# Performance work log

Measured on AMD Instinct MI355X. Metric: run time of the kernel, lower is better.

The kernel has to match this reference:

```python
import jax, jax.numpy as jnp
import numpy as np

EMBED_DIM = 512
NUM_HEADS = 8
HEAD_DIM = EMBED_DIM // NUM_HEADS


def setup_inputs() -> dict:
    key = jax.random.key(0)
    ks = jax.random.split(key, 9)
    C = EMBED_DIM
    s = 1.0 / np.sqrt(C)
    x = jax.random.normal(ks[0], (1, 4096, C), dtype=jnp.float32)
    Wq = jax.random.uniform(ks[1], (C, C), jnp.float32, -s, s)
    bq = jax.random.uniform(ks[2], (C,), jnp.float32, -s, s)
    Wk = jax.random.uniform(ks[3], (C, C), jnp.float32, -s, s)
    bk = jax.random.uniform(ks[4], (C,), jnp.float32, -s, s)
    Wv = jax.random.uniform(ks[5], (C, C), jnp.float32, -s, s)
    bv = jax.random.uniform(ks[6], (C,), jnp.float32, -s, s)
    Wo = jax.random.uniform(ks[7], (C, C), jnp.float32, -s, s)
    bo = jax.random.uniform(ks[8], (C,), jnp.float32, -s, s)
    return {"x": x, "Wq": Wq, "bq": bq, "Wk": Wk, "bk": bk,
            "Wv": Wv, "bv": bv, "Wo": Wo, "bo": bo}


def reference(x, Wq, bq, Wk, bk, Wv, bv, Wo, bo):
    B, N, C = x.shape
    H, D = NUM_HEADS, HEAD_DIM
    # QKV projections, split into heads: [B, H, N, D]
    def proj(W, b):
        y = x @ W + b
        return y.reshape(B, N, H, D).transpose(0, 2, 1, 3)
    Q, K, V = proj(Wq, bq), proj(Wk, bk), proj(Wv, bv)
    # NOTE: original scales by 1/sqrt(embed_dim), NOT 1/sqrt(head_dim)
    scale = 1.0 / jnp.sqrt(jnp.float32(C)).astype(x.dtype)
    scores = jnp.einsum('bhnd,bhmd->bhnm', Q, K) * scale  # [B,H,N,N]
    attn = jax.nn.softmax(scores, axis=-1)
    out = jnp.einsum('bhnm,bhmd->bhnd', attn, V)  # [B,H,N,D]
    out = out.transpose(0, 2, 1, 3).reshape(B, N, C)
    return out @ Wo + bo
```

## Files before the change

kernel.cpp:

```cpp
#include <hip/hip_runtime.h>
#include <hip/hip_bf16.h>

#define SEQ 4096
#define CDIM 512
#define NHEAD 8
#define HDIM 64
#define KVB 64
#define NSPLIT 4
#define TILES_PER_SPLIT (SEQ / KVB / NSPLIT)

typedef __attribute__((ext_vector_type(8))) short bf16x8;
typedef __attribute__((ext_vector_type(4))) float f32x4;
typedef __attribute__((ext_vector_type(16))) float f32x16;

__device__ __forceinline__ short f2b(float f) {
  union { float f; unsigned u; } v; v.f = f;
  unsigned u = v.u;
  unsigned r = u + 0x7fffu + ((u >> 16) & 1u);
  return (short)(r >> 16);
}
__device__ __forceinline__ float b2f(short s) {
  union { unsigned u; float f; } v; v.u = ((unsigned)(unsigned short)s) << 16;
  return v.f;
}
__device__ __forceinline__ unsigned pk2(float a, float b) {
  union { __hip_bfloat162 h; unsigned u; } z;
  z.h = __float22bfloat162_rn(make_float2(a, b));
  return z.u;
}

__global__ __launch_bounds__(256) void prep_kernel(
    const float* __restrict__ x,
    const float* __restrict__ Wq, const float* __restrict__ Wk,
    const float* __restrict__ Wv, const float* __restrict__ Wo,
    short* __restrict__ xb,
    short* __restrict__ Wqt, short* __restrict__ Wkt,
    short* __restrict__ Wvt, short* __restrict__ Wot) {
  __shared__ short tile[32][33];
  int b = blockIdx.x, tid = threadIdx.x;
  if (b < 2048) {
    int i = (b * 256 + tid) * 4;
    float4 v = *(const float4*)(x + i);
    short4 o;
    o.x = f2b(v.x); o.y = f2b(v.y); o.z = f2b(v.z); o.w = f2b(v.w);
    *(short4*)(xb + i) = o;
    return;
  }
  int t = b - 2048;
  int mat = t >> 8; t &= 255;
  const float* W = mat == 0 ? Wq : mat == 1 ? Wk : mat == 2 ? Wv : Wo;
  short* Wt = mat == 0 ? Wqt : mat == 1 ? Wkt : mat == 2 ? Wvt : Wot;
  int n0 = (t & 15) * 32, k0 = (t >> 4) * 32;
  int tx = tid & 31, ty = tid >> 5;
  for (int i = 0; i < 32; i += 8)
    tile[ty + i][tx] = f2b(W[(size_t)(k0 + ty + i) * CDIM + n0 + tx]);
  __syncthreads();
  for (int i = 0; i < 32; i += 8)
    Wt[(size_t)(n0 + ty + i) * CDIM + k0 + tx] = tile[tx][ty + i];
}

__global__ __launch_bounds__(256) void qkv_gemm_kernel(
    const short* __restrict__ A,
    const short* __restrict__ Wqt, const short* __restrict__ Wkt, const short* __restrict__ Wvt,
    const float* __restrict__ bq, const float* __restrict__ bk, const float* __restrict__ bv,
    short* __restrict__ Qb, short* __restrict__ Kb, short* __restrict__ Vtb) {
  __shared__ short As[64 * 64];
  __shared__ short Bs[64 * 64];
  const int z = blockIdx.z;
  const short* Bt = z == 0 ? Wqt : z == 1 ? Wkt : Wvt;
  const float* bias = z == 0 ? bq : z == 1 ? bk : bv;
  const int m0 = blockIdx.x * 64, n0 = blockIdx.y * 64;
  const int tid = threadIdx.x;
  const int w = tid >> 6, lane = tid & 63, g = lane >> 4, l16 = lane & 15;
  f32x4 acc[4] = {};
  for (int kt = 0; kt < CDIM; kt += 64) {
    __syncthreads();
    for (int it = 0; it < 2; ++it) {
      int c = tid + it * 256;
      int r = c >> 3, cc = (c & 7) * 8;
      int sw = r * 64 + (cc ^ ((r & 7) * 8));
      *(bf16x8*)(As + sw) = *(const bf16x8*)(A + (size_t)(m0 + r) * CDIM + kt + cc);
      *(bf16x8*)(Bs + sw) = *(const bf16x8*)(Bt + (size_t)(n0 + r) * CDIM + kt + cc);
    }
    __syncthreads();
    const int ar = w * 16 + l16;
    for (int ks = 0; ks < 2; ++ks) {
      int c0 = ks * 32 + 8 * g;
      bf16x8 af = *(const bf16x8*)(As + ar * 64 + (c0 ^ ((ar & 7) * 8)));
      for (int ni = 0; ni < 4; ++ni) {
        int br = ni * 16 + l16;
        bf16x8 bf = *(const bf16x8*)(Bs + br * 64 + (c0 ^ ((br & 7) * 8)));
        acc[ni] = __builtin_amdgcn_mfma_f32_16x16x32_bf16(af, bf, acc[ni], 0, 0, 0);
      }
    }
  }
  for (int ni = 0; ni < 4; ++ni) {
    int col = n0 + ni * 16 + l16;
    float bv_ = bias[col];
    for (int j = 0; j < 4; ++j) {
      int row = m0 + w * 16 + g * 4 + j;
      float v = acc[ni][j] + bv_;
      if (z == 0)      Qb[(size_t)row * CDIM + col] = f2b(v);
      else if (z == 1) Kb[(size_t)row * CDIM + col] = f2b(v);
      else             Vtb[(size_t)col * SEQ + row] = f2b(v);
    }
  }
}

__global__ __launch_bounds__(256) void out_gemm_kernel(
    const short* __restrict__ A, const short* __restrict__ Bt,
    const float* __restrict__ bias, float* __restrict__ out) {
  __shared__ short As[64 * 64];
  __shared__ short Bs[64 * 64];
  const int m0 = blockIdx.x * 64, n0 = blockIdx.y * 64;
  const int tid = threadIdx.x;
  const int w = tid >> 6, lane = tid & 63, g = lane >> 4, l16 = lane & 15;
  f32x4 acc[4] = {};
  for (int kt = 0; kt < CDIM; kt += 64) {
    __syncthreads();
    for (int it = 0; it < 2; ++it) {
      int c = tid + it * 256;
      int r = c >> 3, cc = (c & 7) * 8;
      int sw = r * 64 + (cc ^ ((r & 7) * 8));
      *(bf16x8*)(As + sw) = *(const bf16x8*)(A + (size_t)(m0 + r) * CDIM + kt + cc);
      *(bf16x8*)(Bs + sw) = *(const bf16x8*)(Bt + (size_t)(n0 + r) * CDIM + kt + cc);
    }
    __syncthreads();
    const int ar = w * 16 + l16;
    for (int ks = 0; ks < 2; ++ks) {
      int c0 = ks * 32 + 8 * g;
      bf16x8 af = *(const bf16x8*)(As + ar * 64 + (c0 ^ ((ar & 7) * 8)));
      for (int ni = 0; ni < 4; ++ni) {
        int br = ni * 16 + l16;
        bf16x8 bf = *(const bf16x8*)(Bs + br * 64 + (c0 ^ ((br & 7) * 8)));
        acc[ni] = __builtin_amdgcn_mfma_f32_16x16x32_bf16(af, bf, acc[ni], 0, 0, 0);
      }
    }
  }
  for (int ni = 0; ni < 4; ++ni) {
    int col = n0 + ni * 16 + l16;
    float bv_ = bias[col];
    for (int j = 0; j < 4; ++j) {
      int row = m0 + w * 16 + g * 4 + j;
      out[(size_t)row * CDIM + col] = acc[ni][j] + bv_;
    }
  }
}

__global__ __launch_bounds__(512, 4) void attn_kernel(
    const short* __restrict__ Qb,
    const short* __restrict__ Kb,
    const short* __restrict__ Vtb,
    short* __restrict__ Op0, short* __restrict__ Op1,
    short* __restrict__ Op2, short* __restrict__ Op3,
    float* __restrict__ lpart) {
  __shared__ __align__(16) char arena[33792];
  __shared__ float lzp[4][32];
  short* KsB = (short*)arena;
  short* VsB = (short*)(arena + 16384);
  const int bid = blockIdx.x;
  const int h = bid & 7;
  const int rest = bid >> 3;
  const int split = rest & 3;
  const int q0 = (rest >> 2) * 128;
  const int kvbase = split * (TILES_PER_SPLIT * KVB);
  const int tid = threadIdx.x;
  const int wid = tid >> 6, lane = tid & 63;
  const int l31 = lane & 31, hi = lane >> 5;
  const int rh = wid >> 1, kq = wid & 1;
  const float scale2 = 0.06375872274f;

  short* Opart = split == 0 ? Op0 : split == 1 ? Op1 : split == 2 ? Op2 : Op3;

  bf16x8 qf[4];
  {
    int qrow = q0 + rh * 32 + l31;
#pragma unroll
    for (int kst = 0; kst < 4; ++kst) {
      bf16x8 q = *(const bf16x8*)(Qb + (size_t)qrow * CDIM + h * 64 + kst * 16 + hi * 8);
#pragma unroll
      for (int i = 0; i < 8; ++i) q[i] = f2b(b2f(q[i]) * scale2);
      qf[kst] = q;
    }
  }

  const int srow = tid >> 3;
  const int scol8 = 8 * ((tid & 7) ^ (srow & 7));
  auto stage = [&](int buf, int kv0) {
    __builtin_amdgcn_global_load_lds(
        (const __attribute__((address_space(1))) void*)(
            Kb + (size_t)(kv0 + srow) * CDIM + h * 64 + scol8),
        (__attribute__((address_space(3))) void*)(&KsB[buf * 4096 + tid * 8]), 16, 0, 0);
    __builtin_amdgcn_global_load_lds(
        (const __attribute__((address_space(1))) void*)(
            Vtb + (size_t)(h * 64 + srow) * SEQ + kv0 + scol8),
        (__attribute__((address_space(3))) void*)(&VsB[buf * 4096 + tid * 8]), 16, 0, 0);
  };

  f32x16 osum[2] = {};
  float lsum = 0.f;

  stage(0, kvbase);
  __syncthreads();

  int cur = 0;
  for (int t = 0; t < TILES_PER_SPLIT; ++t) {
    if (t + 1 < TILES_PER_SPLIT) stage(cur ^ 1, kvbase + (t + 1) * KVB);

    const short* ks_lds = KsB + cur * 4096;
    const short* vs_lds = VsB + cur * 4096;

    f32x16 s = {};
    __builtin_amdgcn_s_setprio(1);
#pragma unroll
    for (int kst = 0; kst < 4; ++kst) {
      int row = kq * 32 + l31;
      bf16x8 kf = *(const bf16x8*)(ks_lds + row * 64 + ((kst * 16 + hi * 8) ^ ((row & 7) * 8)));
      s = __builtin_amdgcn_mfma_f32_32x32x16_bf16(kf, qf[kst], s, 0, 0, 0);
    }
    __builtin_amdgcn_s_setprio(0);

    unsigned w[8];
    float ls0 = 0.f, ls1 = 0.f;
#pragma unroll
    for (int m = 0; m < 8; ++m) {
      float p0 = __builtin_amdgcn_exp2f(s[2 * m]);
      float p1 = __builtin_amdgcn_exp2f(s[2 * m + 1]);
      ls0 += p0; ls1 += p1;
      w[m] = pk2(p0, p1);
    }
    lsum += ls0 + ls1;

#pragma unroll
    for (int ks2 = 0; ks2 < 2; ++ks2) {
      union { unsigned u[4]; bf16x8 v; } pf;
#if __has_builtin(__builtin_amdgcn_permlane32_swap)
      {
        auto sw0 = __builtin_amdgcn_permlane32_swap(w[4 * ks2 + 0], w[4 * ks2 + 2], false, false);
        auto sw1 = __builtin_amdgcn_permlane32_swap(w[4 * ks2 + 1], w[4 * ks2 + 3], false, false);
        pf.u[0] = sw0[0]; pf.u[1] = sw1[0]; pf.u[2] = sw0[1]; pf.u[3] = sw1[1];
      }
#else
      {
        unsigned t0 = hi ? w[4 * ks2 + 0] : w[4 * ks2 + 2];
        unsigned t1 = hi ? w[4 * ks2 + 1] : w[4 * ks2 + 3];
        unsigned r0 = __shfl_xor(t0, 32);
        unsigned r1 = __shfl_xor(t1, 32);
        pf.u[0] = hi ? r0 : w[4 * ks2 + 0];
        pf.u[1] = hi ? r1 : w[4 * ks2 + 1];
        pf.u[2] = hi ? w[4 * ks2 + 2] : r0;
        pf.u[3] = hi ? w[4 * ks2 + 3] : r1;
      }
#endif
      __builtin_amdgcn_s_setprio(1);
#pragma unroll
      for (int dm = 0; dm < 2; ++dm) {
        int vrow = dm * 32 + l31;
        bf16x8 vf = *(const bf16x8*)(
            vs_lds + vrow * 64 + ((kq * 32 + ks2 * 16 + hi * 8) ^ ((vrow & 7) * 8)));
        osum[dm] = __builtin_amdgcn_mfma_f32_32x32x16_bf16(vf, pf.v, osum[dm], 0, 0, 0);
      }
      __builtin_amdgcn_s_setprio(0);
    }

    __syncthreads();
    cur ^= 1;
  }

  lsum += __shfl_xor(lsum, 32);

  __syncthreads();
  float* bufA = (float*)arena;
#define OD(dm, r) ((dm) * 32 + ((r) & 3) + 8 * ((r) >> 2) + 4 * hi)
#define OADDR(dm, r) (rh * 2112 + OD(dm, r) * 33 + l31)
  if (kq == 1) {
    if (hi == 0) lzp[rh][l31] = lsum;
#pragma unroll
    for (int dm = 0; dm < 2; ++dm)
#pragma unroll
      for (int r = 0; r < 16; ++r) bufA[OADDR(dm, r)] = osum[dm][r];
  }
  __syncthreads();
  if (kq == 0) {
#pragma unroll
    for (int dm = 0; dm < 2; ++dm)
#pragma unroll
      for (int r = 0; r < 16; ++r) {
        float v = osum[dm][r] + bufA[OADDR(dm, r)];
        bufA[OADDR(dm, r)] = v;
      }
    float lt = lsum + lzp[rh][l31];
    if (hi == 0)
      lpart[(size_t)(split * NHEAD + h) * SEQ + q0 + rh * 32 + l31] = lt;
  }
  __syncthreads();
#undef OD
#undef OADDR

  {
    int q_ = tid >> 2;
    int dc = (tid & 3) * 16;
    int qr = q_ >> 5, ql = q_ & 31;
    short ov[16];
#pragma unroll
    for (int i = 0; i < 16; ++i)
      ov[i] = f2b(bufA[qr * 2112 + (dc + i) * 33 + ql]);
    *(bf16x8*)(Opart + (size_t)(q0 + q_) * CDIM + h * 64 + dc) = *(bf16x8*)(ov);
    *(bf16x8*)(Opart + (size_t)(q0 + q_) * CDIM + h * 64 + dc + 8) = *(bf16x8*)(ov + 8);
  }
}

__global__ __launch_bounds__(256) void combine_kernel(
    const short* __restrict__ p0, const short* __restrict__ p1,
    const short* __restrict__ p2, const short* __restrict__ p3,
    const float* __restrict__ lpart, short* __restrict__ Ab) {
  int t = blockIdx.x * 256 + threadIdx.x;
  size_t base = (size_t)t * 8;
  int q = (int)(base >> 9), c = (int)(base & 511), h = c >> 6;
  float l = lpart[(size_t)(0 * NHEAD + h) * SEQ + q] +
            lpart[(size_t)(1 * NHEAD + h) * SEQ + q] +
            lpart[(size_t)(2 * NHEAD + h) * SEQ + q] +
            lpart[(size_t)(3 * NHEAD + h) * SEQ + q];
  float rinv = 1.f / l;
  bf16x8 a0 = *(const bf16x8*)(p0 + base);
  bf16x8 a1 = *(const bf16x8*)(p1 + base);
  bf16x8 a2 = *(const bf16x8*)(p2 + base);
  bf16x8 a3 = *(const bf16x8*)(p3 + base);
  short ov[8];
#pragma unroll
  for (int i = 0; i < 8; ++i)
    ov[i] = f2b((b2f(a0[i]) + b2f(a1[i]) + b2f(a2[i]) + b2f(a3[i])) * rinv);
  *(bf16x8*)(Ab + base) = *(bf16x8*)(ov);
}

extern "C" void kernel_launch(void* const* d_in, const int* in_sizes, int n_in,
                              void* d_out, int out_size, void* d_ws, size_t ws_size,
                              hipStream_t stream) {
  const float* x  = (const float*)d_in[0];
  const float* Wq = (const float*)d_in[1];
  const float* bq = (const float*)d_in[2];
  const float* Wk = (const float*)d_in[3];
  const float* bk = (const float*)d_in[4];
  const float* Wv = (const float*)d_in[5];
  const float* bv = (const float*)d_in[6];
  const float* Wo = (const float*)d_in[7];
  const float* bo = (const float*)d_in[8];
  float* out = (float*)d_out;

  short* ws = (short*)d_ws;
  size_t off = 0;
  short* xb  = ws + off; off += (size_t)SEQ * CDIM;
  short* Wqt = ws + off; off += (size_t)CDIM * CDIM;
  short* Wkt = ws + off; off += (size_t)CDIM * CDIM;
  short* Wvt = ws + off; off += (size_t)CDIM * CDIM;
  short* Wot = ws + off; off += (size_t)CDIM * CDIM;
  short* Qb  = ws + off; off += (size_t)SEQ * CDIM;
  short* Kb  = ws + off; off += (size_t)SEQ * CDIM;
  short* Vtb = ws + off; off += (size_t)CDIM * SEQ;
  short* Ab  = ws + off; off += (size_t)SEQ * CDIM;
  short* Op1 = ws + off; off += (size_t)SEQ * CDIM;
  short* Op2 = ws + off; off += (size_t)SEQ * CDIM;
  short* Op3 = ws + off; off += (size_t)SEQ * CDIM;
  float* lpart = (float*)(ws + off); off += (size_t)NSPLIT * NHEAD * SEQ * 2;
  short* Op0 = xb;

  prep_kernel<<<2048 + 4 * 256, 256, 0, stream>>>(x, Wq, Wk, Wv, Wo, xb, Wqt, Wkt, Wvt, Wot);
  qkv_gemm_kernel<<<dim3(SEQ / 64, CDIM / 64, 3), 256, 0, stream>>>(
      xb, Wqt, Wkt, Wvt, bq, bk, bv, Qb, Kb, Vtb);
  attn_kernel<<<(SEQ / 128) * NHEAD * NSPLIT, 512, 0, stream>>>(
      Qb, Kb, Vtb, Op0, Op1, Op2, Op3, lpart);
  combine_kernel<<<SEQ * CDIM / 8 / 256, 256, 0, stream>>>(Op0, Op1, Op2, Op3, lpart, Ab);
  out_gemm_kernel<<<dim3(SEQ / 64, CDIM / 64), 256, 0, stream>>>(Ab, Wot, bo, out);
}
```

Measured before the change: 88.72 us.

## Software-pipeline attention loop: overlap QK^T of next tile with PV of current

Restructures the attention KV loop so that each phase issues the QK^T MFMAs for tile t+1 alongside the PV MFMAs for tile t. The exp2/softmax for the new scores is computed after the MFMAs are issued, so it can overlap with them. This needs K/V staging to move from double to triple LDS buffering, with a prologue that computes the first scores and an epilogue that does the last PV. Staging addresses are now advanced incrementally by pointer bumps instead of being recomputed each time. The larger LDS footprint (48KB arena) may lower the number of resident blocks per CU below the requested four.

```diff
diff --git a/kernel.cpp b/kernel.cpp
--- a/kernel.cpp
+++ b/kernel.cpp
@@ -154,10 +154,10 @@
     short* __restrict__ Op0, short* __restrict__ Op1,
     short* __restrict__ Op2, short* __restrict__ Op3,
     float* __restrict__ lpart) {
-  __shared__ __align__(16) char arena[33792];
+  __shared__ __align__(16) char arena[49152];
   __shared__ float lzp[4][32];
   short* KsB = (short*)arena;
-  short* VsB = (short*)(arena + 16384);
+  short* VsB = (short*)(arena + 24576);
   const int bid = blockIdx.x;
   const int h = bid & 7;
   const int rest = bid >> 3;
@@ -186,41 +186,24 @@
 
   const int srow = tid >> 3;
   const int scol8 = 8 * ((tid & 7) ^ (srow & 7));
-  auto stage = [&](int buf, int kv0) {
+  const short* kstage = Kb + (size_t)(kvbase + srow) * CDIM + h * 64 + scol8;
+  const short* vstage = Vtb + (size_t)(h * 64 + srow) * SEQ + kvbase + scol8;
+  auto stage = [&](short* sK, short* sV) {
     __builtin_amdgcn_global_load_lds(
-        (const __attribute__((address_space(1))) void*)(
-            Kb + (size_t)(kv0 + srow) * CDIM + h * 64 + scol8),
-        (__attribute__((address_space(3))) void*)(&KsB[buf * 4096 + tid * 8]), 16, 0, 0);
+        (const __attribute__((address_space(1))) void*)kstage,
+        (__attribute__((address_space(3))) void*)(sK + tid * 8), 16, 0, 0);
     __builtin_amdgcn_global_load_lds(
-        (const __attribute__((address_space(1))) void*)(
-            Vtb + (size_t)(h * 64 + srow) * SEQ + kv0 + scol8),
-        (__attribute__((address_space(3))) void*)(&VsB[buf * 4096 + tid * 8]), 16, 0, 0);
+        (const __attribute__((address_space(1))) void*)vstage,
+        (__attribute__((address_space(3))) void*)(sV + tid * 8), 16, 0, 0);
+    kstage += KVB * CDIM;
+    vstage += KVB;
   };
 
   f32x16 osum[2] = {};
   float lsum = 0.f;
-
-  stage(0, kvbase);
-  __syncthreads();
-
-  int cur = 0;
-  for (int t = 0; t < TILES_PER_SPLIT; ++t) {
-    if (t + 1 < TILES_PER_SPLIT) stage(cur ^ 1, kvbase + (t + 1) * KVB);
-
-    const short* ks_lds = KsB + cur * 4096;
-    const short* vs_lds = VsB + cur * 4096;
-
-    f32x16 s = {};
-    __builtin_amdgcn_s_setprio(1);
-#pragma unroll
-    for (int kst = 0; kst < 4; ++kst) {
-      int row = kq * 32 + l31;
-      bf16x8 kf = *(const bf16x8*)(ks_lds + row * 64 + ((kst * 16 + hi * 8) ^ ((row & 7) * 8)));
-      s = __builtin_amdgcn_mfma_f32_32x32x16_bf16(kf, qf[kst], s, 0, 0, 0);
-    }
-    __builtin_amdgcn_s_setprio(0);
-
-    unsigned w[8];
+  unsigned w[8];
+
+  auto softmax = [&](f32x16& s) {
     float ls0 = 0.f, ls1 = 0.f;
 #pragma unroll
     for (int m = 0; m < 8; ++m) {
@@ -230,41 +213,101 @@
       w[m] = pk2(p0, p1);
     }
     lsum += ls0 + ls1;
-
-#pragma unroll
-    for (int ks2 = 0; ks2 < 2; ++ks2) {
-      union { unsigned u[4]; bf16x8 v; } pf;
+  };
+
+  auto phase = [&](const short* vbuf, const short* kbuf, short* sK, short* sV, bool do_st) {
+    if (do_st) stage(sK, sV);
+    union { unsigned u[4]; bf16x8 v; } pf0, pf1;
 #if __has_builtin(__builtin_amdgcn_permlane32_swap)
-      {
-        auto sw0 = __builtin_amdgcn_permlane32_swap(w[4 * ks2 + 0], w[4 * ks2 + 2], false, false);
-        auto sw1 = __builtin_amdgcn_permlane32_swap(w[4 * ks2 + 1], w[4 * ks2 + 3], false, false);
-        pf.u[0] = sw0[0]; pf.u[1] = sw1[0]; pf.u[2] = sw0[1]; pf.u[3] = sw1[1];
-      }
+    {
+      auto a0 = __builtin_amdgcn_permlane32_swap(w[0], w[2], false, false);
+      auto a1 = __builtin_amdgcn_permlane32_swap(w[1], w[3], false, false);
+      auto a2 = __builtin_amdgcn_permlane32_swap(w[4], w[6], false, false);
+      auto a3 = __builtin_amdgcn_permlane32_swap(w[5], w[7], false, false);
+      pf0.u[0] = a0[0]; pf0.u[1] = a1[0]; pf0.u[2] = a0[1]; pf0.u[3] = a1[1];
+      pf1.u[0] = a2[0]; pf1.u[1] = a3[0]; pf1.u[2] = a2[1]; pf1.u[3] = a3[1];
+    }
 #else
-      {
-        unsigned t0 = hi ? w[4 * ks2 + 0] : w[4 * ks2 + 2];
-        unsigned t1 = hi ? w[4 * ks2 + 1] : w[4 * ks2 + 3];
-        unsigned r0 = __shfl_xor(t0, 32);
-        unsigned r1 = __shfl_xor(t1, 32);
-        pf.u[0] = hi ? r0 : w[4 * ks2 + 0];
-        pf.u[1] = hi ? r1 : w[4 * ks2 + 1];
-        pf.u[2] = hi ? w[4 * ks2 + 2] : r0;
-        pf.u[3] = hi ? w[4 * ks2 + 3] : r1;
-      }
+    {
+      unsigned t0 = hi ? w[0] : w[2], t1 = hi ? w[1] : w[3];
+      unsigned t2 = hi ? w[4] : w[6], t3 = hi ? w[5] : w[7];
+      unsigned r0 = __shfl_xor(t0, 32), r1 = __shfl_xor(t1, 32);
+      unsigned r2 = __shfl_xor(t2, 32), r3 = __shfl_xor(t3, 32);
+      pf0.u[0] = hi ? r0 : w[0]; pf0.u[1] = hi ? r1 : w[1];
+      pf0.u[2] = hi ? w[2] : r0; pf0.u[3] = hi ? w[3] : r1;
+      pf1.u[0] = hi ? r2 : w[4]; pf1.u[1] = hi ? r3 : w[5];
+      pf1.u[2] = hi ? w[6] : r2; pf1.u[3] = hi ? w[7] : r3;
+    }
 #endif
-      __builtin_amdgcn_s_setprio(1);
-#pragma unroll
-      for (int dm = 0; dm < 2; ++dm) {
-        int vrow = dm * 32 + l31;
-        bf16x8 vf = *(const bf16x8*)(
-            vs_lds + vrow * 64 + ((kq * 32 + ks2 * 16 + hi * 8) ^ ((vrow & 7) * 8)));
-        osum[dm] = __builtin_amdgcn_mfma_f32_32x32x16_bf16(vf, pf.v, osum[dm], 0, 0, 0);
-      }
-      __builtin_amdgcn_s_setprio(0);
-    }
-
+    f32x16 s = {};
+    __builtin_amdgcn_s_setprio(1);
+#pragma unroll
+    for (int kst = 0; kst < 4; ++kst) {
+      int row = kq * 32 + l31;
+      bf16x8 kf = *(const bf16x8*)(kbuf + row * 64 + ((kst * 16 + hi * 8) ^ ((row & 7) * 8)));
+      s = __builtin_amdgcn_mfma_f32_32x32x16_bf16(kf, qf[kst], s, 0, 0, 0);
+    }
+#pragma unroll
+    for (int dm = 0; dm < 2; ++dm) {
+      int vrow = dm * 32 + l31;
+      bf16x8 vf0 = *(const bf16x8*)(vbuf + vrow * 64 + ((kq * 32 + hi * 8) ^ ((vrow & 7) * 8)));
+      osum[dm] = __builtin_amdgcn_mfma_f32_32x32x16_bf16(vf0, pf0.v, osum[dm], 0, 0, 0);
+      bf16x8 vf1 = *(const bf16x8*)(vbuf + vrow * 64 + ((kq * 32 + 16 + hi * 8) ^ ((vrow & 7) * 8)));
+      osum[dm] = __builtin_amdgcn_mfma_f32_32x32x16_bf16(vf1, pf1.v, osum[dm], 0, 0, 0);
+    }
+    __builtin_amdgcn_s_setprio(0);
+    softmax(s);
     __syncthreads();
-    cur ^= 1;
+  };
+
+  stage(KsB, VsB);
+  __syncthreads();
+  stage(KsB + 4096, VsB + 4096);
+  {
+    f32x16 s = {};
+#pragma unroll
+    for (int kst = 0; kst < 4; ++kst) {
+      int row = kq * 32 + l31;
+      bf16x8 kf = *(const bf16x8*)(KsB + row * 64 + ((kst * 16 + hi * 8) ^ ((row & 7) * 8)));
+      s = __builtin_amdgcn_mfma_f32_32x32x16_bf16(kf, qf[kst], s, 0, 0, 0);
+    }
+    softmax(s);
+  }
+  __syncthreads();
+
+  for (int t = 0; t < TILES_PER_SPLIT - 1; t += 3) {
+    phase(VsB,        KsB + 4096, KsB + 8192, VsB + 8192, t + 2 < TILES_PER_SPLIT);
+    phase(VsB + 4096, KsB + 8192, KsB,        VsB,        t + 3 < TILES_PER_SPLIT);
+    phase(VsB + 8192, KsB,        KsB + 4096, VsB + 4096, t + 4 < TILES_PER_SPLIT);
+  }
+
+  {
+    union { unsigned u[4]; bf16x8 v; } pf0, pf1;
+#if __has_builtin(__builtin_amdgcn_permlane32_swap)
+    auto a0 = __builtin_amdgcn_permlane32_swap(w[0], w[2], false, false);
+    auto a1 = __builtin_amdgcn_permlane32_swap(w[1], w[3], false, false);
+    auto a2 = __builtin_amdgcn_permlane32_swap(w[4], w[6], false, false);
+    auto a3 = __builtin_amdgcn_permlane32_swap(w[5], w[7], false, false);
+    pf0.u[0] = a0[0]; pf0.u[1] = a1[0]; pf0.u[2] = a0[1]; pf0.u[3] = a1[1];
+    pf1.u[0] = a2[0]; pf1.u[1] = a3[0]; pf1.u[2] = a2[1]; pf1.u[3] = a3[1];
+#else
+    unsigned t0 = hi ? w[0] : w[2], t1 = hi ? w[1] : w[3];
+    unsigned t2 = hi ? w[4] : w[6], t3 = hi ? w[5] : w[7];
+    unsigned r0 = __shfl_xor(t0, 32), r1 = __shfl_xor(t1, 32);
+    unsigned r2 = __shfl_xor(t2, 32), r3 = __shfl_xor(t3, 32);
+    pf0.u[0] = hi ? r0 : w[0]; pf0.u[1] = hi ? r1 : w[1];
+    pf0.u[2] = hi ? w[2] : r0; pf0.u[3] = hi ? w[3] : r1;
+    pf1.u[0] = hi ? r2 : w[4]; pf1.u[1] = hi ? r3 : w[5];
+    pf1.u[2] = hi ? w[6] : r2; pf1.u[3] = hi ? w[7] : r3;
+#endif
+#pragma unroll
+    for (int dm = 0; dm < 2; ++dm) {
+      int vrow = dm * 32 + l31;
+      bf16x8 vf0 = *(const bf16x8*)(VsB + vrow * 64 + ((kq * 32 + hi * 8) ^ ((vrow & 7) * 8)));
+      osum[dm] = __builtin_amdgcn_mfma_f32_32x32x16_bf16(vf0, pf0.v, osum[dm], 0, 0, 0);
+      bf16x8 vf1 = *(const bf16x8*)(VsB + vrow * 64 + ((kq * 32 + 16 + hi * 8) ^ ((vrow & 7) * 8)));
+      osum[dm] = __builtin_amdgcn_mfma_f32_32x32x16_bf16(vf1, pf1.v, osum[dm], 0, 0, 0);
+    }
   }
 
   lsum += __shfl_xor(lsum, 32);
```

After: 87.46 us. Within noise of the previous version (-1.4%).
